# Performance work log

Measured on AMD Instinct MI355X. Metric: run time of the kernel, lower is better.

Reference implementation:

```python
import jax, jax.numpy as jnp
import numpy as np

N = 1000; K = 500; M = N - K          # codeword / info / parity bits
NUE = 4; NBS = 4                      # tx / rx antennas
BPS = 4; RATE = 0.5; NSYM = N // BPS  # 16-QAM, 250 symbols per codeword
NITER = 5                             # BP iterations

# 16-QAM constellation, Gray-coded per axis (Sionna-style), unit energy
_bits = ((np.arange(16)[:, None] >> np.array([3, 2, 1, 0])) & 1).astype(np.float32)
_re = (1 - 2 * _bits[:, 0]) * (2 - (1 - 2 * _bits[:, 2]))
_im = (1 - 2 * _bits[:, 1]) * (2 - (1 - 2 * _bits[:, 3]))
POINTS = jnp.asarray((_re + 1j * _im) / np.sqrt(10.0), dtype=jnp.complex64)  # [16]
LABELS = jnp.asarray(_bits)  # [16,4] bit labels per point


def setup_inputs() -> dict:
    key = jax.random.key(0)
    ks = jax.random.split(key, 5)
    batch = 1000
    # systematic sparse LDPC-like code: H = [P^T | I_M], info-bit degree 3
    rs = np.random.RandomState(0)
    P = np.zeros((K, M), np.int32)
    for i in range(K):
        P[i, rs.choice(M, 3, replace=False)] = 1
    vi, ci = np.nonzero(P)
    vn = np.concatenate([vi, K + np.arange(M)]).astype(np.int32)  # [2000]
    cn = np.concatenate([ci, np.arange(M)]).astype(np.int32)      # [2000]
    b = jax.random.randint(ks[0], (batch, NUE, K), 0, 2, dtype=jnp.int32)
    h_re = jax.random.normal(ks[1], (batch * NSYM, NBS, NUE), jnp.float32)
    h_im = jax.random.normal(ks[2], (batch * NSYM, NBS, NUE), jnp.float32)
    n_re = jax.random.normal(ks[3], (batch * NSYM, NBS), jnp.float32)
    n_im = jax.random.normal(ks[4], (batch * NSYM, NBS), jnp.float32)
    return {"batch_size": batch, "ebno_db": jnp.full((1,), 5.0, jnp.float32),
            "b": b, "P": jnp.asarray(P), "cn_idx": jnp.asarray(cn),
            "vn_idx": jnp.asarray(vn), "h_re": h_re, "h_im": h_im,
            "noise_re": n_re, "noise_im": n_im}


def _forward(batch_size, ebno_db, b, P, cn_idx, vn_idx, h_re, h_im, noise_re, noise_im):
    no = 1.0 / (10.0 ** (ebno_db[0] / 10.0) * BPS * RATE)  # ebnodb2no
    # --- LDPC encode (systematic): c = [b, b@P mod 2] ---
    bf = b.astype(jnp.float32)
    parity = jnp.mod(jnp.round(bf @ P.astype(jnp.float32)), 2.0)
    c = jnp.concatenate([bf, parity], -1)                    # [B,NUE,N]
    # --- QAM mapper ---
    idx = (c.reshape(batch_size, NUE, NSYM, BPS) @ jnp.array([8., 4., 2., 1.], jnp.float32)).astype(jnp.int32)
    x = POINTS[idx]                                          # [B,NUE,NSYM]
    x_f = jnp.transpose(x, (0, 2, 1)).reshape(-1, NUE)       # [B*NSYM,NUE]
    # --- flat fading channel, h ~ CN(0,1), AWGN ---
    h = ((h_re + 1j * h_im) / np.sqrt(2.0)).astype(jnp.complex64)
    w = ((noise_re + 1j * noise_im) * jnp.sqrt(no / 2.0)).astype(jnp.complex64)
    y = jnp.einsum('bij,bj->bi', h, x_f) + w                 # [B*NSYM,NBS]
    # --- LMMSE equalizer: G = H^H (H H^H + no I)^-1, unbiased scaling ---
    A = jnp.einsum('bik,bjk->bij', h, jnp.conj(h)) \
        + no.astype(jnp.complex64) * jnp.eye(NBS, dtype=jnp.complex64)
    Ainv_y = jnp.linalg.solve(A, y[..., None])[..., 0]
    x_raw = jnp.einsum('bij,bi->bj', jnp.conj(h), Ainv_y)    # G y, [B*NSYM,NUE]
    GH = jnp.einsum('bij,bik->bjk', jnp.conj(h), jnp.linalg.solve(A, h))
    d = jnp.real(jnp.diagonal(GH, axis1=1, axis2=2))         # diag(GH), [B*NSYM,NUE]
    x_hat = x_raw / d.astype(jnp.complex64)
    no_eff = jnp.maximum(1.0 / d - 1.0, 1e-12)
    x_hat = jnp.transpose(x_hat.reshape(batch_size, NSYM, NUE), (0, 2, 1))  # [B,NUE,NSYM]
    nvar = jnp.transpose(no_eff.reshape(batch_size, NSYM, NUE), (0, 2, 1))
    # --- max-log demapper, L = log p(b=0)/p(b=1) ---
    metric = -(jnp.abs(x_hat[..., None] - POINTS) ** 2) / nvar[..., None]   # [B,NUE,NSYM,16]
    NEG = jnp.float32(-1e30)
    m5 = metric[..., None, :]                               # [B,NUE,NSYM,1,16]
    lab = LABELS.T[None, None, None]                        # [1,1,1,4,16]
    m0 = jnp.max(jnp.where(lab == 0, m5, NEG), -1)
    m1 = jnp.max(jnp.where(lab == 1, m5, NEG), -1)
    llr = (m0 - m1).reshape(batch_size, NUE, N)
    # --- LDPC BP decoder (sum-product over fixed sparse Tanner graph) ---
    Lch = llr.reshape(batch_size * NUE, N).T                # [N, Bc]
    c2v = jnp.zeros((cn_idx.shape[0], Lch.shape[1]), jnp.float32)  # [E, Bc]
    for _ in range(NITER):
        vtot = Lch.at[vn_idx].add(c2v)                      # Lch + segment_sum(c2v)
        m_vc = vtot[vn_idx] - c2v                           # extrinsic VN->CN
        t = jnp.tanh(jnp.clip(m_vc * 0.5, -9.9, 9.9))
        t = jnp.where(t >= 0, jnp.maximum(t, 1e-7), jnp.minimum(t, -1e-7))
        prod = jax.ops.segment_prod(t, cn_idx, num_segments=M)
        c2v = 2.0 * jnp.arctanh(jnp.clip(prod[cn_idx] / t, -0.999999, 0.999999))
    vtot = Lch.at[vn_idx].add(c2v)
    b_hat = (vtot[:K].T < 0).astype(jnp.float32).reshape(batch_size, NUE, K)
    return bf, b_hat


def reference(batch_size, ebno_db, b, P, cn_idx, vn_idx, h_re, h_im, noise_re, noise_im):
    return _forward(batch_size, ebno_db, b, P, cn_idx, vn_idx,
                    h_re, h_im, noise_re, noise_im)
```

## Files before the change

kernel.cpp:

```cpp
#include <hip/hip_runtime.h>
#include <math.h>

#define KK     500
#define MM     500
#define NNODES 1000
#define NSYM   250
#define NITERS 5
#define MAXVDEG 4
#define EMAX   2048
#define TB     512

#define SWZ(s) ((s) ^ (((s) >> 4) & 3))

__global__ void __launch_bounds__(512)
k_setup(const int* __restrict__ cn, const int* __restrict__ vn, int E,
        const float* __restrict__ ebno, const int* __restrict__ P,
        const int* __restrict__ b, int ncw,
        int* __restrict__ cinfo, int* __restrict__ vlist, int* __restrict__ coff,
        int* __restrict__ cdend, int* __restrict__ cperm,
        double* __restrict__ nobuf, unsigned* __restrict__ Ppack,
        unsigned* __restrict__ bpack, float* __restrict__ out, int packBlocks) {
  __shared__ int sdeg[512];
  __shared__ int scinv[512];
  __shared__ int sdnew[512];
  __shared__ int sexcl[512];
  __shared__ int ssc[512];
  __shared__ int scur[512];
  __shared__ int svc[NNODES];
  __shared__ int shist[64];
  __shared__ int shcur[64];
  int tid = threadIdx.x;
  int bx = blockIdx.x;

  if (bx == 0) {
    sdeg[tid] = 0;
    for (int n = tid; n < NNODES; n += 512) svc[n] = 0;
    if (tid < 64) { shist[tid] = 0; shcur[tid] = 0; }
    __syncthreads();
    for (int e = tid; e < E; e += 512) atomicAdd(&sdeg[cn[e]], 1);
    __syncthreads();
    int d = (tid < MM) ? sdeg[tid] : 0;
    if (tid < MM) atomicAdd(&shist[d], 1);
    __syncthreads();
    if (tid == 0) {
      int acc = 0;
      for (int i = 0; i < 64; ++i) { int h = shist[i]; shist[i] = acc; shcur[i] = acc; acc += h; }
    }
    __syncthreads();
    if (tid < MM) {
      int nid = atomicAdd(&shcur[d], 1);
      scinv[tid] = nid;
      cperm[nid] = tid;
      sdnew[nid] = d;
    }
    __syncthreads();
    int v = (tid < MM) ? sdnew[tid] : 0;
    ssc[tid] = v;
    __syncthreads();
    for (int o = 1; o < 512; o <<= 1) {
      int x = (tid >= o) ? ssc[tid - o] : 0;
      __syncthreads();
      ssc[tid] += x;
      __syncthreads();
    }
    int excl = ssc[tid] - v;
    sexcl[tid] = excl;
    scur[tid] = excl;
    if (tid < MM) {
      coff[tid]  = excl;
      cdend[tid] = excl + sdnew[tid] - 1;
      if (tid == MM - 1) coff[MM] = ssc[tid];
    }
    __syncthreads();
    for (int e = tid; e < E; e += 512) {
      int c = cn[e], n = vn[e];
      int nc = scinv[c];
      int slot;
      if (n >= KK) {
        slot = sexcl[nc] + sdeg[c] - 1;
      } else {
        slot = atomicAdd(&scur[nc], 1);
      }
      cinfo[slot] = (nc << 16) | n;
      if (n < KK) {
        int t = atomicAdd(&svc[n], 1);
        if (t < MAXVDEG) vlist[n * MAXVDEG + t] = slot;
      }
    }
    if (tid == 0) {
      double no = 1.0 / (pow(10.0, (double)ebno[0] * 0.1) * 2.0);
      nobuf[0] = no;
      nobuf[1] = sqrt(no * 0.5);
    }
    return;
  }

  if (bx <= packBlocks) {
    int id = (bx - 1) * 512 + tid;
    if (id < MM * 16) {
      int j = id >> 4, w = id & 15;
      unsigned word = 0u;
      int base = w * 32;
      for (int bit = 0; bit < 32; ++bit) {
        int i = base + bit;
        if (i < KK && P[i * MM + j] != 0) word |= (1u << bit);
      }
      Ppack[j * 16 + w] = word;
    } else {
      int id2 = id - MM * 16;
      if (id2 < ncw * 16) {
        int cw = id2 >> 4, w = id2 & 15;
        unsigned word = 0u;
        int base = w * 32;
        for (int bit = 0; bit < 32; ++bit) {
          int i = base + bit;
          if (i < KK && b[cw * KK + i] != 0) word |= (1u << bit);
        }
        bpack[cw * 16 + w] = word;
      }
    }
    return;
  }

  int id = (bx - 1 - packBlocks) * 512 + tid;
  if (id < ncw * KK) out[id] = (float)b[id];
}

__device__ __forceinline__ void qam_pointf(int p, float& re, float& im) {
  const float s = 0.31622776601683794f;
  int b0 = (p >> 3) & 1, b1 = (p >> 2) & 1, b2 = (p >> 1) & 1, b3 = p & 1;
  re = (float)((1 - 2 * b0) * (2 - (1 - 2 * b2))) * s;
  im = (float)((1 - 2 * b1) * (2 - (1 - 2 * b3))) * s;
}

__device__ __forceinline__ float tanh_half(float m) {
  float mc = fminf(fmaxf(m, -19.8f), 19.8f);
  float e = __expf(mc);
  float t = 1.0f - __fdividef(2.0f, e + 1.0f);
  return (t >= 0.0f) ? fmaxf(t, 1e-7f) : fminf(t, -1e-7f);
}
__device__ __forceinline__ float4 tanh_half4(float4 m) {
  return make_float4(tanh_half(m.x), tanh_half(m.y), tanh_half(m.z), tanh_half(m.w));
}
__device__ __forceinline__ float pclip(float P, float t) {
  return copysignf(fminf(fabsf(P), 0.999999f * fabsf(t)), P);
}
__device__ __forceinline__ float tfloor(float t) {
  return (t >= 0.0f) ? fmaxf(t, 1e-7f) : fminf(t, -1e-7f);
}
__device__ __forceinline__ float atanh2c(float P, float t) {
  float r = __fdividef(P, t);
  r = fminf(fmaxf(r, -0.999999f), 0.999999f);
  return __logf(__fdividef(1.0f + r, 1.0f - r));
}

#define SOLVE_DEMAP(J, Lout) {                                                          \
  float u0r = Hr[0][J] * i00,               u0i = Hi[0][J] * i00;                       \
  float u1r = (Hr[1][J] - (L10r * u0r - L10i * u0i)) * i11;                             \
  float u1i = (Hi[1][J] - (L10r * u0i + L10i * u0r)) * i11;                             \
  float u2r = (Hr[2][J] - (L20r * u0r - L20i * u0i) - (L21r * u1r - L21i * u1i)) * i22; \
  float u2i = (Hi[2][J] - (L20r * u0i + L20i * u0r) - (L21r * u1i + L21i * u1r)) * i22; \
  float u3r = (Hr[3][J] - (L30r * u0r - L30i * u0i) - (L31r * u1r - L31i * u1i)         \
                        - (L32r * u2r - L32i * u2i)) * i33;                             \
  float u3i = (Hi[3][J] - (L30r * u0i + L30i * u0r) - (L31r * u1i + L31i * u1r)         \
                        - (L32r * u2i + L32i * u2r)) * i33;                             \
  float dj = (u0r * u0r + u0i * u0i) + (u1r * u1r + u1i * u1i)                          \
           + (u2r * u2r + u2i * u2i) + (u3r * u3r + u3i * u3i);                         \
  float rr = (u0r * yr[0] + u0i * yi[0]) + (u1r * yr[1] + u1i * yi[1])                  \
           + (u2r * yr[2] + u2i * yi[2]) + (u3r * yr[3] + u3i * yi[3]);                 \
  float ri = (u0r * yi[0] - u0i * yr[0]) + (u1r * yi[1] - u1i * yr[1])                  \
           + (u2r * yi[2] - u2i * yr[2]) + (u3r * yi[3] - u3i * yr[3]);                 \
  float rdj = __fdividef(1.0f, dj);                                                    \
  float xhr = rr * rdj, xhi = ri * rdj;                                                \
  float gap = 1.0f - dj;                                                               \
  float inoe = __fdividef(dj, fmaxf(gap, dj * 1e-12f));                                \
  float m0[4] = {-1e30f, -1e30f, -1e30f, -1e30f};                                      \
  float m1[4] = {-1e30f, -1e30f, -1e30f, -1e30f};                                      \
  _Pragma("unroll")                                                                    \
  for (int p = 0; p < 16; ++p) {                                                       \
    float dr = xhr - PRT[p], di = xhi - PIT[p];                                        \
    float met = -(dr * dr + di * di) * inoe;                                           \
    _Pragma("unroll")                                                                  \
    for (int k = 0; k < 4; ++k) {                                                      \
      if ((p >> (3 - k)) & 1) m1[k] = fmaxf(m1[k], met);                               \
      else                    m0[k] = fmaxf(m0[k], met);                               \
    }                                                                                  \
  }                                                                                    \
  _Pragma("unroll")                                                                    \
  for (int k = 0; k < 4; ++k) Lout[k] = m0[k] - m1[k];                                 \
}

#define VUPD(C) {                                                                      \
  float p0 = pclip(P0.C, t0.C), p1 = pclip(P1.C, t1.C), p2 = pclip(P2.C, t2.C);        \
  float a0 = t0.C + p0, a1 = t1.C + p1, a2 = t2.C + p2;                                \
  float b0 = t0.C - p0, b1 = t1.C - p1, b2 = t2.C - p2;                                \
  float Ec = En.C;                                                                     \
  float A0 = Ec * (a1 * a2), A1 = Ec * (a0 * a2), A2 = Ec * (a0 * a1);                 \
  float B0 = b1 * b2,        B1 = b0 * b2,        B2 = b0 * b1;                        \
  n0.C = tfloor(__fdividef(A0 - B0, A0 + B0));                                         \
  n1.C = tfloor(__fdividef(A1 - B1, A1 + B1));                                         \
  n2.C = tfloor(__fdividef(A2 - B2, A2 + B2));                                         \
}

__global__ void __launch_bounds__(512, 4)
k_fused(const float* __restrict__ h_re, const float* __restrict__ h_im,
        const float* __restrict__ n_re, const float* __restrict__ n_im,
        const double* __restrict__ nobuf,
        const unsigned* __restrict__ bpack, const unsigned* __restrict__ Ppack,
        const int* __restrict__ vlist, const int* __restrict__ coff,
        const int* __restrict__ cdend, const int* __restrict__ cperm,
        const int* __restrict__ cinfo, float* __restrict__ out, int ncw) {
  __shared__ float4 sT[EMAX];
  __shared__ float4 sP[512];
  float4* sL = sT;

  int tid = threadIdx.x;
  int bt = blockIdx.x;

  if (tid < NSYM) {
    int t = bt * NSYM + tid;
    int s = tid;

    float no = (float)nobuf[0];
    float sq = (float)nobuf[1];
    const float is2 = 0.70710678118654752f;

    float Hr[4][4], Hi[4][4];
    {
      const float4* hr4 = (const float4*)h_re;
      const float4* hi4 = (const float4*)h_im;
      #pragma unroll
      for (int i = 0; i < 4; ++i) {
        float4 a = hr4[t * 4 + i], c = hi4[t * 4 + i];
        Hr[i][0] = a.x * is2; Hr[i][1] = a.y * is2;
        Hr[i][2] = a.z * is2; Hr[i][3] = a.w * is2;
        Hi[i][0] = c.x * is2; Hi[i][1] = c.y * is2;
        Hi[i][2] = c.z * is2; Hi[i][3] = c.w * is2;
      }
    }

    float xr[4], xi[4];
    #pragma unroll
    for (int ue = 0; ue < 4; ++ue) {
      const unsigned* bp = bpack + (bt * 4 + ue) * 16;
      int v = 0;
      #pragma unroll
      for (int k = 0; k < 4; ++k) {
        int n = 4 * s + k;
        int bit;
        if (n < KK) {
          bit = (bp[n >> 5] >> (n & 31)) & 1;
        } else {
          const unsigned* pp = Ppack + (n - KK) * 16;
          int cnt = 0;
          #pragma unroll
          for (int w = 0; w < 16; ++w) cnt += __popc(bp[w] & pp[w]);
          bit = cnt & 1;
        }
        v = (v << 1) | bit;
      }
      qam_pointf(v, xr[ue], xi[ue]);
    }

    float yr[4], yi[4];
    {
      float4 wr = ((const float4*)n_re)[t];
      float4 wi = ((const float4*)n_im)[t];
      float wrv[4] = {wr.x, wr.y, wr.z, wr.w};
      float wiv[4] = {wi.x, wi.y, wi.z, wi.w};
      #pragma unroll
      for (int i = 0; i < 4; ++i) {
        float ar = wrv[i] * sq;
        float ai = wiv[i] * sq;
        #pragma unroll
        for (int j = 0; j < 4; ++j) {
          ar += Hr[i][j] * xr[j] - Hi[i][j] * xi[j];
          ai += Hr[i][j] * xi[j] + Hi[i][j] * xr[j];
        }
        yr[i] = ar; yi[i] = ai;
      }
    }

    auto dotc = [&](int i, int j, float& ar, float& ai) {
      float r = 0.0f, m = 0.0f;
      #pragma unroll
      for (int k = 0; k < 4; ++k) {
        r += Hr[i][k] * Hr[j][k] + Hi[i][k] * Hi[j][k];
        m += Hi[i][k] * Hr[j][k] - Hr[i][k] * Hi[j][k];
      }
      ar = r; ai = m;
    };
    float a00, a11, a22, a33, dum;
    float a10r, a10i, a20r, a20i, a21r, a21i, a30r, a30i, a31r, a31i, a32r, a32i;
    dotc(0, 0, a00, dum);  a00 += no;
    dotc(1, 0, a10r, a10i);
    dotc(1, 1, a11, dum);  a11 += no;
    dotc(2, 0, a20r, a20i);
    dotc(2, 1, a21r, a21i);
    dotc(2, 2, a22, dum);  a22 += no;
    dotc(3, 0, a30r, a30i);
    dotc(3, 1, a31r, a31i);
    dotc(3, 2, a32r, a32i);
    dotc(3, 3, a33, dum);  a33 += no;

    float i00 = rsqrtf(a00);
    float L10r = a10r * i00, L10i = a10i * i00;
    float L20r = a20r * i00, L20i = a20i * i00;
    float L30r = a30r * i00, L30i = a30i * i00;
    float d11 = a11 - (L10r * L10r + L10i * L10i);
    float i11 = rsqrtf(d11);
    float L21r = (a21r - (L20r * L10r + L20i * L10i)) * i11;
    float L21i = (a21i - (L20i * L10r - L20r * L10i)) * i11;
    float L31r = (a31r - (L30r * L10r + L30i * L10i)) * i11;
    float L31i = (a31i - (L30i * L10r - L30r * L10i)) * i11;
    float d22 = a22 - (L20r * L20r + L20i * L20i) - (L21r * L21r + L21i * L21i);
    float i22 = rsqrtf(d22);
    float L32r = (a32r - (L30r * L20r + L30i * L20i) - (L31r * L21r + L31i * L21i)) * i22;
    float L32i = (a32i - (L30i * L20r - L30r * L20i) - (L31i * L21r - L31r * L21i)) * i22;
    float d33 = a33 - (L30r * L30r + L30i * L30i) - (L31r * L31r + L31i * L31i)
                    - (L32r * L32r + L32i * L32i);
    float i33 = rsqrtf(d33);

    {
      float v0r = yr[0] * i00,               v0i = yi[0] * i00;
      float v1r = (yr[1] - (L10r * v0r - L10i * v0i)) * i11;
      float v1i = (yi[1] - (L10r * v0i + L10i * v0r)) * i11;
      float v2r = (yr[2] - (L20r * v0r - L20i * v0i) - (L21r * v1r - L21i * v1i)) * i22;
      float v2i = (yi[2] - (L20r * v0i + L20i * v0r) - (L21r * v1i + L21i * v1r)) * i22;
      float v3r = (yr[3] - (L30r * v0r - L30i * v0i) - (L31r * v1r - L31i * v1i)
                         - (L32r * v2r - L32i * v2i)) * i33;
      float v3i = (yi[3] - (L30r * v0i + L30i * v0r) - (L31r * v1i + L31i * v1r)
                         - (L32r * v2i + L32i * v2r)) * i33;
      yr[0] = v0r; yi[0] = v0i; yr[1] = v1r; yi[1] = v1i;
      yr[2] = v2r; yi[2] = v2i; yr[3] = v3r; yi[3] = v3i;
    }

    const float PRT[16] = { 0.31622776601683794f, 0.31622776601683794f, 0.9486832980505138f, 0.9486832980505138f,
                            0.31622776601683794f, 0.31622776601683794f, 0.9486832980505138f, 0.9486832980505138f,
                           -0.31622776601683794f,-0.31622776601683794f,-0.9486832980505138f,-0.9486832980505138f,
                           -0.31622776601683794f,-0.31622776601683794f,-0.9486832980505138f,-0.9486832980505138f };
    const float PIT[16] = { 0.31622776601683794f, 0.9486832980505138f, 0.31622776601683794f, 0.9486832980505138f,
                           -0.31622776601683794f,-0.9486832980505138f,-0.31622776601683794f,-0.9486832980505138f,
                            0.31622776601683794f, 0.9486832980505138f, 0.31622776601683794f, 0.9486832980505138f,
                           -0.31622776601683794f,-0.9486832980505138f,-0.31622776601683794f,-0.9486832980505138f };

    float l0[4], l1[4], l2[4], l3[4];
    SOLVE_DEMAP(0, l0);
    SOLVE_DEMAP(1, l1);
    SOLVE_DEMAP(2, l2);
    SOLVE_DEMAP(3, l3);
    #pragma unroll
    for (int k = 0; k < 4; ++k) {
      sL[4 * s + k] = make_float4(l0[k], l1[k], l2[k], l3[k]);
    }
  }
  __syncthreads();

  int n = tid;
  bool iok = n < KK;
  float4 Ln = make_float4(0.f, 0.f, 0.f, 0.f);
  float4 En = make_float4(1.f, 1.f, 1.f, 1.f);
  int pk0 = 0, pk1 = 0, pk2 = 0;
  if (iok) {
    float4 L = sL[n];
    Ln = L;
    En = make_float4(__expf(fminf(fmaxf(L.x, -55.f), 55.f)),
                     __expf(fminf(fmaxf(L.y, -55.f), 55.f)),
                     __expf(fminf(fmaxf(L.z, -55.f), 55.f)),
                     __expf(fminf(fmaxf(L.w, -55.f), 55.f)));
    int s0 = vlist[n * MAXVDEG], s1 = vlist[n * MAXVDEG + 1], s2 = vlist[n * MAXVDEG + 2];
    pk0 = (cinfo[s0] & 0xffff0000) | SWZ(s0);
    pk1 = (cinfo[s1] & 0xffff0000) | SWZ(s1);
    pk2 = (cinfo[s2] & 0xffff0000) | SWZ(s2);
  }
  bool cok = tid < MM;
  float4 qpar = make_float4(1.f, 1.f, 1.f, 1.f);
  int beg = 0, dnd = 0;
  if (cok) {
    int oc = cperm[tid];
    qpar = tanh_half4(sL[KK + oc]);
    beg = coff[tid];
    dnd = cdend[tid];
  }
  __syncthreads();

  for (int it = 0; it < NITERS; ++it) {
    if (it == 0) {
      if (iok) {
        float4 t = tanh_half4(Ln);
        sT[pk0 & 0xffff] = t;
        sT[pk1 & 0xffff] = t;
        sT[pk2 & 0xffff] = t;
      }
    } else {
      if (iok) {
        int s0 = pk0 & 0xffff, c0 = ((unsigned)pk0) >> 16;
        int s1 = pk1 & 0xffff, c1 = ((unsigned)pk1) >> 16;
        int s2 = pk2 & 0xffff, c2 = ((unsigned)pk2) >> 16;
        float4 P0 = sP[c0], P1 = sP[c1], P2 = sP[c2];
        float4 t0 = sT[s0], t1 = sT[s1], t2 = sT[s2];
        float4 n0, n1, n2;
        VUPD(x); VUPD(y); VUPD(z); VUPD(w);
        sT[s0] = n0;
        sT[s1] = n1;
        sT[s2] = n2;
      }
    }
    __syncthreads();
    if (cok) {
      float4 p = qpar;
      for (int e = beg; e < dnd; ++e) {
        float4 tt = sT[SWZ(e)];
        p.x *= tt.x; p.y *= tt.y; p.z *= tt.z; p.w *= tt.w;
      }
      sP[tid] = p;
    }
    __syncthreads();
  }

  int cw0 = bt * 4;
  float* o0 = out + (size_t)ncw * KK + (size_t)cw0 * KK;
  float* o1 = o0 + KK;
  float* o2 = o1 + KK;
  float* o3 = o2 + KK;
  if (iok) {
    int s0 = pk0 & 0xffff, c0 = ((unsigned)pk0) >> 16;
    int s1 = pk1 & 0xffff, c1 = ((unsigned)pk1) >> 16;
    int s2 = pk2 & 0xffff, c2 = ((unsigned)pk2) >> 16;
    float4 P0 = sP[c0], P1 = sP[c1], P2 = sP[c2];
    float4 t0 = sT[s0], t1 = sT[s1], t2 = sT[s2];
    float4 L = Ln;
    float ax = L.x + atanh2c(P0.x, t0.x) + atanh2c(P1.x, t1.x) + atanh2c(P2.x, t2.x);
    float ay = L.y + atanh2c(P0.y, t0.y) + atanh2c(P1.y, t1.y) + atanh2c(P2.y, t2.y);
    float az = L.z + atanh2c(P0.z, t0.z) + atanh2c(P1.z, t1.z) + atanh2c(P2.z, t2.z);
    float aw = L.w + atanh2c(P0.w, t0.w) + atanh2c(P1.w, t1.w) + atanh2c(P2.w, t2.w);
    o0[n] = (ax < 0.0f) ? 1.0f : 0.0f;
    o1[n] = (ay < 0.0f) ? 1.0f : 0.0f;
    o2[n] = (az < 0.0f) ? 1.0f : 0.0f;
    o3[n] = (aw < 0.0f) ? 1.0f : 0.0f;
  }
}

extern "C" void kernel_launch(void* const* d_in, const int* in_sizes, int n_in,
                              void* d_out, int out_size, void* d_ws, size_t ws_size,
                              hipStream_t stream) {
  const float* ebno = (const float*)d_in[1];
  const int*   b    = (const int*)d_in[2];
  const int*   P    = (const int*)d_in[3];
  const int*   cn   = (const int*)d_in[4];
  const int*   vn   = (const int*)d_in[5];
  const float* h_re = (const float*)d_in[6];
  const float* h_im = (const float*)d_in[7];
  const float* nre  = (const float*)d_in[8];
  const float* nim  = (const float*)d_in[9];
  float* out = (float*)d_out;

  int E     = in_sizes[4];
  int batch = in_sizes[2] / (4 * KK);
  int ncw   = batch * 4;

  char* ws = (char*)d_ws;
  size_t off = 0;
  auto alloc = [&](size_t bytes) -> void* {
    void* p = ws + off;
    off += (bytes + 255) & ~(size_t)255;
    return p;
  };
  unsigned* Ppack  = (unsigned*)alloc((size_t)MM * 16 * 4);
  unsigned* bpack  = (unsigned*)alloc((size_t)ncw * 16 * 4);
  int*      coff   = (int*)alloc((size_t)(MM + 1) * 4);
  int*      cdend  = (int*)alloc((size_t)MM * 4);
  int*      cperm  = (int*)alloc((size_t)MM * 4);
  int*      cinfo  = (int*)alloc((size_t)EMAX * 4);
  int*      vlist  = (int*)alloc((size_t)NNODES * MAXVDEG * 4);
  double*   nobuf  = (double*)alloc(2 * 8);
  (void)ws_size; (void)n_in; (void)out_size;

  int packItems  = MM * 16 + ncw * 16;
  int packBlocks = (packItems + 511) / 512;
  int bfBlocks   = (ncw * KK + 511) / 512;
  int setupGrid  = 1 + packBlocks + bfBlocks;

  k_setup<<<dim3(setupGrid), dim3(512), 0, stream>>>(cn, vn, E, ebno, P, b, ncw,
                                                     cinfo, vlist, coff, cdend, cperm,
                                                     nobuf, Ppack, bpack, out, packBlocks);
  k_fused<<<dim3(batch), dim3(512), 0, stream>>>(h_re, h_im, nre, nim, nobuf,
                                                 bpack, Ppack, vlist, coff, cdend,
                                                 cperm, cinfo, out, ncw);
}
```

Measured before the change: 168.3 us.

## Split each fused block's four user codewords into two blocks of two

After: 192.9 us. 14.6% more time.

```diff
diff --git a/kernel.cpp b/kernel.cpp
--- a/kernel.cpp
+++ b/kernel.cpp
@@ -138,9 +138,6 @@
   float e = __expf(mc);
   float t = 1.0f - __fdividef(2.0f, e + 1.0f);
   return (t >= 0.0f) ? fmaxf(t, 1e-7f) : fminf(t, -1e-7f);
-}
-__device__ __forceinline__ float4 tanh_half4(float4 m) {
-  return make_float4(tanh_half(m.x), tanh_half(m.y), tanh_half(m.z), tanh_half(m.w));
 }
 __device__ __forceinline__ float pclip(float P, float t) {
   return copysignf(fminf(fabsf(P), 0.999999f * fabsf(t)), P);
@@ -190,7 +187,7 @@
   for (int k = 0; k < 4; ++k) Lout[k] = m0[k] - m1[k];                                 \
 }
 
-#define VUPD(C) {                                                                      \
+#define VUPD2(C) {                                                                     \
   float p0 = pclip(P0.C, t0.C), p1 = pclip(P1.C, t1.C), p2 = pclip(P2.C, t2.C);        \
   float a0 = t0.C + p0, a1 = t1.C + p1, a2 = t2.C + p2;                                \
   float b0 = t0.C - p0, b1 = t1.C - p1, b2 = t2.C - p2;                                \
@@ -210,12 +207,13 @@
         const int* __restrict__ vlist, const int* __restrict__ coff,
         const int* __restrict__ cdend, const int* __restrict__ cperm,
         const int* __restrict__ cinfo, float* __restrict__ out, int ncw) {
-  __shared__ float4 sT[EMAX];
-  __shared__ float4 sP[512];
-  float4* sL = sT;
+  __shared__ float2 sT[EMAX];
+  __shared__ float2 sP[512];
+  float2* sL = sT;
 
   int tid = threadIdx.x;
-  int bt = blockIdx.x;
+  int pairId = blockIdx.x;
+  int bt = pairId >> 1, plane = pairId & 1;
 
   if (tid < NSYM) {
     int t = bt * NSYM + tid;
@@ -344,41 +342,43 @@
                             0.31622776601683794f, 0.9486832980505138f, 0.31622776601683794f, 0.9486832980505138f,
                            -0.31622776601683794f,-0.9486832980505138f,-0.31622776601683794f,-0.9486832980505138f };
 
-    float l0[4], l1[4], l2[4], l3[4];
-    SOLVE_DEMAP(0, l0);
-    SOLVE_DEMAP(1, l1);
-    SOLVE_DEMAP(2, l2);
-    SOLVE_DEMAP(3, l3);
+    float lA[4], lB[4];
+    if (plane == 0) {
+      SOLVE_DEMAP(0, lA);
+      SOLVE_DEMAP(1, lB);
+    } else {
+      SOLVE_DEMAP(2, lA);
+      SOLVE_DEMAP(3, lB);
+    }
     #pragma unroll
     for (int k = 0; k < 4; ++k) {
-      sL[4 * s + k] = make_float4(l0[k], l1[k], l2[k], l3[k]);
+      sL[4 * s + k] = make_float2(lA[k], lB[k]);
     }
   }
   __syncthreads();
 
   int n = tid;
   bool iok = n < KK;
-  float4 Ln = make_float4(0.f, 0.f, 0.f, 0.f);
-  float4 En = make_float4(1.f, 1.f, 1.f, 1.f);
+  float2 Ln = make_float2(0.f, 0.f);
+  float2 En = make_float2(1.f, 1.f);
   int pk0 = 0, pk1 = 0, pk2 = 0;
   if (iok) {
-    float4 L = sL[n];
+    float2 L = sL[n];
     Ln = L;
-    En = make_float4(__expf(fminf(fmaxf(L.x, -55.f), 55.f)),
-                     __expf(fminf(fmaxf(L.y, -55.f), 55.f)),
-                     __expf(fminf(fmaxf(L.z, -55.f), 55.f)),
-                     __expf(fminf(fmaxf(L.w, -55.f), 55.f)));
+    En = make_float2(__expf(fminf(fmaxf(L.x, -55.f), 55.f)),
+                     __expf(fminf(fmaxf(L.y, -55.f), 55.f)));
     int s0 = vlist[n * MAXVDEG], s1 = vlist[n * MAXVDEG + 1], s2 = vlist[n * MAXVDEG + 2];
     pk0 = (cinfo[s0] & 0xffff0000) | SWZ(s0);
     pk1 = (cinfo[s1] & 0xffff0000) | SWZ(s1);
     pk2 = (cinfo[s2] & 0xffff0000) | SWZ(s2);
   }
   bool cok = tid < MM;
-  float4 qpar = make_float4(1.f, 1.f, 1.f, 1.f);
+  float2 qpar = make_float2(1.f, 1.f);
   int beg = 0, dnd = 0;
   if (cok) {
     int oc = cperm[tid];
-    qpar = tanh_half4(sL[KK + oc]);
+    float2 Lp = sL[KK + oc];
+    qpar = make_float2(tanh_half(Lp.x), tanh_half(Lp.y));
     beg = coff[tid];
     dnd = cdend[tid];
   }
@@ -387,7 +387,7 @@
   for (int it = 0; it < NITERS; ++it) {
     if (it == 0) {
       if (iok) {
-        float4 t = tanh_half4(Ln);
+        float2 t = make_float2(tanh_half(Ln.x), tanh_half(Ln.y));
         sT[pk0 & 0xffff] = t;
         sT[pk1 & 0xffff] = t;
         sT[pk2 & 0xffff] = t;
@@ -397,10 +397,10 @@
         int s0 = pk0 & 0xffff, c0 = ((unsigned)pk0) >> 16;
         int s1 = pk1 & 0xffff, c1 = ((unsigned)pk1) >> 16;
         int s2 = pk2 & 0xffff, c2 = ((unsigned)pk2) >> 16;
-        float4 P0 = sP[c0], P1 = sP[c1], P2 = sP[c2];
-        float4 t0 = sT[s0], t1 = sT[s1], t2 = sT[s2];
-        float4 n0, n1, n2;
-        VUPD(x); VUPD(y); VUPD(z); VUPD(w);
+        float2 P0 = sP[c0], P1 = sP[c1], P2 = sP[c2];
+        float2 t0 = sT[s0], t1 = sT[s1], t2 = sT[s2];
+        float2 n0, n1, n2;
+        VUPD2(x); VUPD2(y);
         sT[s0] = n0;
         sT[s1] = n1;
         sT[s2] = n2;
@@ -408,36 +408,30 @@
     }
     __syncthreads();
     if (cok) {
-      float4 p = qpar;
+      float2 p = qpar;
       for (int e = beg; e < dnd; ++e) {
-        float4 tt = sT[SWZ(e)];
-        p.x *= tt.x; p.y *= tt.y; p.z *= tt.z; p.w *= tt.w;
+        float2 tt = sT[SWZ(e)];
+        p.x *= tt.x; p.y *= tt.y;
       }
       sP[tid] = p;
     }
     __syncthreads();
   }
 
-  int cw0 = bt * 4;
+  int cw0 = pairId * 2;
   float* o0 = out + (size_t)ncw * KK + (size_t)cw0 * KK;
   float* o1 = o0 + KK;
-  float* o2 = o1 + KK;
-  float* o3 = o2 + KK;
   if (iok) {
     int s0 = pk0 & 0xffff, c0 = ((unsigned)pk0) >> 16;
     int s1 = pk1 & 0xffff, c1 = ((unsigned)pk1) >> 16;
     int s2 = pk2 & 0xffff, c2 = ((unsigned)pk2) >> 16;
-    float4 P0 = sP[c0], P1 = sP[c1], P2 = sP[c2];
-    float4 t0 = sT[s0], t1 = sT[s1], t2 = sT[s2];
-    float4 L = Ln;
+    float2 P0 = sP[c0], P1 = sP[c1], P2 = sP[c2];
+    float2 t0 = sT[s0], t1 = sT[s1], t2 = sT[s2];
+    float2 L = Ln;
     float ax = L.x + atanh2c(P0.x, t0.x) + atanh2c(P1.x, t1.x) + atanh2c(P2.x, t2.x);
     float ay = L.y + atanh2c(P0.y, t0.y) + atanh2c(P1.y, t1.y) + atanh2c(P2.y, t2.y);
-    float az = L.z + atanh2c(P0.z, t0.z) + atanh2c(P1.z, t1.z) + atanh2c(P2.z, t2.z);
-    float aw = L.w + atanh2c(P0.w, t0.w) + atanh2c(P1.w, t1.w) + atanh2c(P2.w, t2.w);
     o0[n] = (ax < 0.0f) ? 1.0f : 0.0f;
     o1[n] = (ay < 0.0f) ? 1.0f : 0.0f;
-    o2[n] = (az < 0.0f) ? 1.0f : 0.0f;
-    o3[n] = (aw < 0.0f) ? 1.0f : 0.0f;
   }
 }
 
@@ -484,7 +478,7 @@
   k_setup<<<dim3(setupGrid), dim3(512), 0, stream>>>(cn, vn, E, ebno, P, b, ncw,
                                                      cinfo, vlist, coff, cdend, cperm,
                                                      nobuf, Ppack, bpack, out, packBlocks);
-  k_fused<<<dim3(batch), dim3(512), 0, stream>>>(h_re, h_im, nre, nim, nobuf,
-                                                 bpack, Ppack, vlist, coff, cdend,
-                                                 cperm, cinfo, out, ncw);
-}
+  k_fused<<<dim3(ncw / 2), dim3(512), 0, stream>>>(h_re, h_im, nre, nim, nobuf,
+                                                   bpack, Ppack, vlist, coff, cdend,
+                                                   cperm, cinfo, out, ncw);
+}
```
